# Optimization experiments

Hardware: AMD Instinct MI355X
Metric: run time of the kernel (lower is better)

Reference implementation:

```python
import jax, jax.numpy as jnp
import numpy as np

L = 6          # n_layers
V = 512        # vocab_size
D = 768        # n_embd == d_model
P = 768        # proj_size
H = 12         # num_heads
HD = P // H    # head dim = 64
FF = 4 * D     # MLP hidden = 3072
BLOCK = 1024   # block_size
B, T = 8, 1024
LN_EPS = 1e-5


def _layernorm(x, g, b):
    mu = jnp.mean(x, axis=-1, keepdims=True)
    var = jnp.mean(jnp.square(x - mu), axis=-1, keepdims=True)
    return (x - mu) * jax.lax.rsqrt(var + LN_EPS) * g + b


def setup_inputs() -> dict:
    key = jax.random.key(0)
    ks = iter(jax.random.split(key, 32))
    s = 0.02

    def rn(shape):
        return (jax.random.normal(next(ks), shape, jnp.float32) * s)

    inp = {
        "idx": jax.random.randint(next(ks), (B, T), 0, V),
        "attn_mask": jnp.ones((B, T), jnp.float32),
        "tok_emb": rn((V, D)),
        "pos_emb": rn((1, BLOCK, D)),
        # per-layer params stacked on leading L axis
        "ln1_g": jnp.ones((L, D)), "ln1_b": jnp.zeros((L, D)),
        "Wq": rn((L, D, P)), "bq": jnp.zeros((L, P)),
        "Wk": rn((L, D, P)), "bk": jnp.zeros((L, P)),
        "Wv": rn((L, D, P)), "bv": jnp.zeros((L, P)),
        "Wo": rn((L, P, D)), "bo": jnp.zeros((L, D)),
        "ln2_g": jnp.ones((L, D)), "ln2_b": jnp.zeros((L, D)),
        "W1": rn((L, D, FF)), "b1": jnp.zeros((L, FF)),
        "W2": rn((L, FF, D)), "b2": jnp.zeros((L, D)),
        "lnf_g": jnp.ones((D,)), "lnf_b": jnp.zeros((D,)),
        "W_out": rn((D, V)),  # logits head, no bias
    }
    return inp


def reference(idx, attn_mask, tok_emb, pos_emb, ln1_g, ln1_b, Wq, bq, Wk, bk,
              Wv, bv, Wo, bo, ln2_g, ln2_b, W1, b1, W2, b2, lnf_g, lnf_b, W_out):
    Bc, Tc = idx.shape
    x = tok_emb[idx] + pos_emb[:, :Tc]  # [B,T,D]  (dropout: eval mode, identity)

    tril = jnp.tril(jnp.ones((Tc, Tc), jnp.float32))
    # torch.minimum(look_ahead_mask, attn_mask.view(B,1,1,T))
    mask = jnp.minimum(tril[None, None], attn_mask[:, None, None, :])  # [B,1,T,T]
    neg_mask = mask == 0
    scale = 1.0 / np.sqrt(HD)

    layer_params = {
        "ln1_g": ln1_g, "ln1_b": ln1_b, "Wq": Wq, "bq": bq, "Wk": Wk, "bk": bk,
        "Wv": Wv, "bv": bv, "Wo": Wo, "bo": bo, "ln2_g": ln2_g, "ln2_b": ln2_b,
        "W1": W1, "b1": b1, "W2": W2, "b2": b2,
    }

    def block(x, p):
        h = _layernorm(x, p["ln1_g"], p["ln1_b"])
        q = (h @ p["Wq"] + p["bq"]).reshape(Bc, Tc, H, HD)
        k = (h @ p["Wk"] + p["bk"]).reshape(Bc, Tc, H, HD)
        v = (h @ p["Wv"] + p["bv"]).reshape(Bc, Tc, H, HD)
        att = jnp.einsum("bqhd,bkhd->bhqk", q, k) * scale
        att = jnp.where(neg_mask, -jnp.inf, att)
        w = jax.nn.softmax(att, axis=-1)  # attn dropout: identity in eval
        y = jnp.einsum("bhqk,bkhd->bqhd", w, v).reshape(Bc, Tc, P)
        x = x + (y @ p["Wo"] + p["bo"])
        h2 = _layernorm(x, p["ln2_g"], p["ln2_b"])
        m = jax.nn.gelu(h2 @ p["W1"] + p["b1"], approximate=False) @ p["W2"] + p["b2"]
        return x + m

    def step(x, p):
        return block(x, p), None

    x, _ = jax.lax.scan(step, x, layer_params)
    x = _layernorm(x, lnf_g, lnf_b)
    logits = x @ W_out  # [B,T,V]
    return logits
```

## Files before the change

### kernel.cpp

```cpp
#include <hip/hip_runtime.h>
#include <stdint.h>

#define LY 6
#define VOC 512
#define DM 768
#define NH 12
#define HD 64
#define FFD 3072
#define BB 8
#define TT 1024
#define ROWS (BB*TT)

typedef short bf16x8 __attribute__((ext_vector_type(8)));
typedef float f32x4 __attribute__((ext_vector_type(4)));
typedef unsigned short u16x4 __attribute__((ext_vector_type(4)));

__device__ __forceinline__ unsigned short f2bf(float f) {
    union { float f; uint32_t u; } v; v.f = f;
    uint32_t r = v.u + 0x7FFFu + ((v.u >> 16) & 1u);
    return (unsigned short)(r >> 16);
}

__device__ __forceinline__ void gl2lds16(const void* g, void* lds) {
    __builtin_amdgcn_global_load_lds(
        (const __attribute__((address_space(1))) uint32_t*)g,
        (__attribute__((address_space(3))) uint32_t*)lds,
        16, 0, 0);
}

__global__ void transpose_w(const float* __restrict__ src, unsigned short* __restrict__ dst,
                            int K, int N, long sls, long dls, int noff) {
    src += (long)blockIdx.z * sls;
    dst += (long)blockIdx.z * dls;
    const int k0 = blockIdx.y * 32, n0 = blockIdx.x * 32;
    __shared__ float tile[32][33];
    const int tx = threadIdx.x, ty = threadIdx.y;
#pragma unroll
    for (int i = 0; i < 4; ++i)
        tile[ty*4+i][tx] = src[(long)(k0 + ty*4 + i) * N + n0 + tx];
    __syncthreads();
#pragma unroll
    for (int i = 0; i < 4; ++i)
        dst[(long)(noff + n0 + ty*4 + i) * K + k0 + tx] = f2bf(tile[tx][ty*4+i]);
}

__global__ void pack_bqkv(const float* __restrict__ bq, const float* __restrict__ bk,
                          const float* __restrict__ bv, float* __restrict__ dst) {
    int i = blockIdx.x * 256 + threadIdx.x;
    if (i >= LY * 2304) return;
    int l = i / 2304, c = i % 2304;
    const float* s = (c < 768) ? bq : (c < 1536 ? bk : bv);
    dst[i] = s[l * 768 + (c % 768)];
}

__global__ __launch_bounds__(256) void embed_kernel(const int* __restrict__ idx,
        const float* __restrict__ tok, const float* __restrict__ pos, float* __restrict__ x) {
    const int g = blockIdx.x * 256 + threadIdx.x;
    const int row = g / 192, c = (g % 192) * 4;
    const int t = row & (TT - 1);
    const int tk = idx[row];
    const f32x4 a = *(const f32x4*)(tok + (long)tk * DM + c);
    const f32x4 p = *(const f32x4*)(pos + (long)t * DM + c);
    f32x4 o = a + p;
    *(f32x4*)(x + (long)row * DM + c) = o;
}

__global__ __launch_bounds__(256) void ln_kernel(const float* __restrict__ x,
        const float* __restrict__ gg, const float* __restrict__ bb,
        unsigned short* __restrict__ out) {
    const int row = (blockIdx.x * 256 + threadIdx.x) >> 6;
    const int lane = threadIdx.x & 63;
    const float* xr = x + (long)row * DM;
    f32x4 v[3];
#pragma unroll
    for (int i = 0; i < 3; ++i) v[i] = *(const f32x4*)(xr + i * 256 + lane * 4);
    float s = 0.f;
#pragma unroll
    for (int i = 0; i < 3; ++i) s += v[i][0] + v[i][1] + v[i][2] + v[i][3];
#pragma unroll
    for (int m = 1; m < 64; m <<= 1) s += __shfl_xor(s, m);
    const float mu = s * (1.f / 768.f);
    float q = 0.f;
#pragma unroll
    for (int i = 0; i < 3; ++i)
#pragma unroll
        for (int j = 0; j < 4; ++j) { float d = v[i][j] - mu; q += d * d; }
#pragma unroll
    for (int m = 1; m < 64; m <<= 1) q += __shfl_xor(q, m);
    const float rs = rsqrtf(q * (1.f / 768.f) + 1e-5f);
#pragma unroll
    for (int i = 0; i < 3; ++i) {
        u16x4 o;
#pragma unroll
        for (int j = 0; j < 4; ++j) {
            const int c = i * 256 + lane * 4 + j;
            o[j] = f2bf((v[i][j] - mu) * rs * gg[c] + bb[c]);
        }
        *(u16x4*)(out + (long)row * DM + i * 256 + lane * 4) = o;
    }
}

template <int EP>
__global__ __launch_bounds__(256)
void gemm128(const unsigned short* __restrict__ A, const unsigned short* __restrict__ Bt,
             const float* __restrict__ bias, const float* __restrict__ res,
             void* __restrict__ Cout, int M, int N, int K,
             unsigned short* __restrict__ aux) {
    __shared__ alignas(16) short As[128 * 64];
    __shared__ alignas(16) short Bs[128 * 64];
    const int tid = threadIdx.x;
    const int w = tid >> 6, lane = tid & 63, quad = lane >> 4, r = lane & 15;
    const int wm = w >> 1, wn = w & 1;
    const long rb = (long)blockIdx.x * 128;
    const long cb = (long)blockIdx.y * 128;

    f32x4 acc[4][4];
    const f32x4 z4 = {0.f, 0.f, 0.f, 0.f};
#pragma unroll
    for (int i = 0; i < 4; ++i)
#pragma unroll
        for (int j = 0; j < 4; ++j) acc[i][j] = z4;

    const int lrow = lane >> 3;
    const int lblk = (lane & 7) ^ lrow;

    for (int k0 = 0; k0 < K; k0 += 64) {
#pragma unroll
        for (int i = 0; i < 4; ++i) {
            const int c = i * 4 + w;
            gl2lds16(A + (rb + 8 * c + lrow) * (long)K + k0 + lblk * 8, (char*)As + c * 1024);
            gl2lds16(Bt + (cb + 8 * c + lrow) * (long)K + k0 + lblk * 8, (char*)Bs + c * 1024);
        }
        __builtin_amdgcn_s_waitcnt(0);
        __syncthreads();
#pragma unroll
        for (int kk = 0; kk < 2; ++kk) {
            bf16x8 af[4], bfr[4];
#pragma unroll
            for (int mi = 0; mi < 4; ++mi) {
                const int row = wm * 64 + mi * 16 + r;
                af[mi] = *(const bf16x8*)((const char*)As + row * 128 + (((kk * 4 + quad) ^ (row & 7)) * 16));
            }
#pragma unroll
            for (int ni = 0; ni < 4; ++ni) {
                const int col = wn * 64 + ni * 16 + r;
                bfr[ni] = *(const bf16x8*)((const char*)Bs + col * 128 + (((kk * 4 + quad) ^ (col & 7)) * 16));
            }
#pragma unroll
            for (int mi = 0; mi < 4; ++mi)
#pragma unroll
                for (int ni = 0; ni < 4; ++ni)
                    acc[mi][ni] = __builtin_amdgcn_mfma_f32_16x16x32_bf16(af[mi], bfr[ni], acc[mi][ni], 0, 0, 0);
        }
        __syncthreads();
    }

    if (EP == 4 && cb >= 1536) {
#pragma unroll
        for (int ni = 0; ni < 4; ++ni) {
            const int col = (int)cb + wn * 64 + ni * 16 + r;
            const float bv = bias[col];
            const int c = col - 1536, hh = c >> 6, dd = c & 63;
#pragma unroll
            for (int mi = 0; mi < 4; ++mi) {
                const int row0 = (int)rb + wm * 64 + mi * 16 + quad * 4;
                const int bb2 = row0 >> 10, t = row0 & 1023;
                u16x4 o;
#pragma unroll
                for (int reg = 0; reg < 4; ++reg) o[reg] = f2bf(acc[mi][ni][reg] + bv);
                *(u16x4*)(aux + (long)((bb2 * NH + hh) * 64 + dd) * TT + t) = o;
            }
        }
        return;
    }

#pragma unroll
    for (int ni = 0; ni < 4; ++ni) {
        const long col = cb + wn * 64 + ni * 16 + r;
        const float bv = (EP == 3) ? 0.f : bias[col];
#pragma unroll
        for (int mi = 0; mi < 4; ++mi) {
            const long row0 = rb + wm * 64 + mi * 16 + quad * 4;
#pragma unroll
            for (int reg = 0; reg < 4; ++reg) {
                const long off = (row0 + reg) * (long)N + col;
                float v = acc[mi][ni][reg] + bv;
                if (EP == 0 || EP == 4) {
                    ((unsigned short*)Cout)[off] = f2bf(v);
                } else if (EP == 1) {
                    v = 0.5f * v * (1.f + erff(v * 0.70710678118654752f));
                    ((unsigned short*)Cout)[off] = f2bf(v);
                } else if (EP == 2) {
                    ((float*)Cout)[off] = res[off] + v;
                } else {
                    ((float*)Cout)[off] = v;
                }
            }
        }
    }
}

__global__ __launch_bounds__(256)
void attn_kernel(const unsigned short* __restrict__ qkv, const unsigned short* __restrict__ vT,
                 const float* __restrict__ amask, unsigned short* __restrict__ y) {
    const int b = blockIdx.z, h = blockIdx.y, qb = blockIdx.x;
    const int q0 = qb * 128;
    const int tid = threadIdx.x, w = tid >> 6, lane = tid & 63, quad = lane >> 4, r = lane & 15;

    __shared__ alignas(16) short Ks[128 * 64];
    __shared__ alignas(16) short Vt[64 * 128];
    __shared__ alignas(16) short Pw[4][16 * 128];
    __shared__ float Msk[128];

    const float NINF = -__builtin_inff();
    const f32x4 z4 = {0.f, 0.f, 0.f, 0.f};

    bf16x8 qf[2][2];
#pragma unroll
    for (int qs = 0; qs < 2; ++qs)
#pragma unroll
        for (int ks = 0; ks < 2; ++ks)
            qf[qs][ks] = *(const bf16x8*)(qkv + (long)(b * TT + q0 + w * 32 + qs * 16 + r) * 2304
                                          + h * 64 + ks * 32 + quad * 8);

    f32x4 acc[2][4];
    float m_i[2] = {NINF, NINF}, l_i[2] = {0.f, 0.f};
#pragma unroll
    for (int qs = 0; qs < 2; ++qs)
#pragma unroll
        for (int dt = 0; dt < 4; ++dt) acc[qs][dt] = z4;

    short* Pme = &Pw[w][0];

    for (int kt = 0; kt <= qb; ++kt) {
#pragma unroll
        for (int i = 0; i < 4; ++i) {
            const int row = w * 32 + i * 8 + (lane >> 3);
            gl2lds16(qkv + (long)(b * TT + kt * 128 + row) * 2304 + 768 + h * 64
                         + (((lane & 7) ^ (row & 7)) << 3),
                     (char*)Ks + (w * 32 + i * 8) * 128);
        }
#pragma unroll
        for (int i = 0; i < 4; ++i) {
            const int drow = w * 16 + i * 4 + (lane >> 4);
            gl2lds16(vT + (long)((b * NH + h) * 64 + drow) * TT + kt * 128
                        + (((lane & 15) ^ (drow & 7)) << 3),
                     (char*)Vt + (w * 16 + i * 4) * 256);
        }
        if (tid < 128) Msk[tid] = amask[b * TT + kt * 128 + tid];
        __builtin_amdgcn_s_waitcnt(0);
        __syncthreads();

        const bool diag = (kt == qb);

        f32x4 s[2][8];
#pragma unroll
        for (int nt = 0; nt < 8; ++nt) {
            s[0][nt] = z4; s[1][nt] = z4;
#pragma unroll
            for (int ks = 0; ks < 2; ++ks) {
                const int krow = nt * 16 + r;
                const bf16x8 kf = *(const bf16x8*)((const char*)Ks + krow * 128
                                     + ((((ks << 2) + quad) ^ (krow & 7)) << 4));
                s[0][nt] = __builtin_amdgcn_mfma_f32_16x16x32_bf16(kf, qf[0][ks], s[0][nt], 0, 0, 0);
                s[1][nt] = __builtin_amdgcn_mfma_f32_16x16x32_bf16(kf, qf[1][ks], s[1][nt], 0, 0, 0);
            }
        }

#pragma unroll
        for (int qs = 0; qs < 2; ++qs) {
            const int qg = q0 + w * 32 + qs * 16 + r;
#pragma unroll
            for (int nt = 0; nt < 8; ++nt) {
                const f32x4 mk4 = *(const f32x4*)(Msk + nt * 16 + quad * 4);
#pragma unroll
                for (int reg = 0; reg < 4; ++reg) {
                    const int key = kt * 128 + nt * 16 + quad * 4 + reg;
                    const bool ok = (mk4[reg] != 0.f) && (!diag || key <= qg);
                    if (!ok) s[qs][nt][reg] = NINF;
                }
            }
            float mx = NINF;
#pragma unroll
            for (int nt = 0; nt < 8; ++nt)
                mx = fmaxf(mx, fmaxf(fmaxf(s[qs][nt][0], s[qs][nt][1]),
                                     fmaxf(s[qs][nt][2], s[qs][nt][3])));
            mx = fmaxf(mx, __shfl_xor(mx, 16));
            mx = fmaxf(mx, __shfl_xor(mx, 32));
            const float mnew = fmaxf(m_i[qs], mx);
            const float alpha = (m_i[qs] == NINF) ? 0.f : __expf((m_i[qs] - mnew) * 0.125f);
            m_i[qs] = mnew;

            float rs = 0.f;
#pragma unroll
            for (int nt = 0; nt < 8; ++nt) {
                u16x4 pk;
#pragma unroll
                for (int reg = 0; reg < 4; ++reg) {
                    const float p = (s[qs][nt][reg] == NINF)
                                  ? 0.f : __expf((s[qs][nt][reg] - mnew) * 0.125f);
                    rs += p;
                    pk[reg] = f2bf(p);
                }
                const int kblk = nt * 2 + (quad >> 1);
                *(u16x4*)(Pme + r * 128 + ((kblk ^ (r & 7)) << 3) + ((quad & 1) << 2)) = pk;
            }
            rs += __shfl_xor(rs, 16);
            rs += __shfl_xor(rs, 32);
            l_i[qs] = l_i[qs] * alpha + rs;

            float al[4];
#pragma unroll
            for (int reg = 0; reg < 4; ++reg)
                al[reg] = __shfl(alpha, (lane & 48) + quad * 4 + reg);
#pragma unroll
            for (int dt = 0; dt < 4; ++dt)
#pragma unroll
                for (int reg = 0; reg < 4; ++reg)
                    acc[qs][dt][reg] *= al[reg];

#pragma unroll
            for (int kk = 0; kk < 4; ++kk) {
                const bf16x8 pf = *(const bf16x8*)(Pme + r * 128
                                     + ((((kk << 2) + quad) ^ (r & 7)) << 3));
#pragma unroll
                for (int dt = 0; dt < 4; ++dt) {
                    const int dd = dt * 16 + r;
                    const bf16x8 vf = *(const bf16x8*)((const char*)Vt + dd * 256
                                        + ((((kk << 2) + quad) ^ (dd & 7)) << 4));
                    acc[qs][dt] = __builtin_amdgcn_mfma_f32_16x16x32_bf16(pf, vf, acc[qs][dt], 0, 0, 0);
                }
            }
        }
        __syncthreads();
    }

#pragma unroll
    for (int qs = 0; qs < 2; ++qs) {
        const float inv0 = 1.0f / l_i[qs];
#pragma unroll
        for (int reg = 0; reg < 4; ++reg) {
            const float inv = __shfl(inv0, (lane & 48) + quad * 4 + reg);
            const long row = b * TT + q0 + w * 32 + qs * 16 + quad * 4 + reg;
#pragma unroll
            for (int dt = 0; dt < 4; ++dt)
                y[row * DM + h * 64 + dt * 16 + r] = f2bf(acc[qs][dt][reg] * inv);
        }
    }
}

extern "C" void kernel_launch(void* const* d_in, const int* in_sizes, int n_in,
                              void* d_out, int out_size, void* d_ws, size_t ws_size,
                              hipStream_t stream) {
    (void)in_sizes; (void)n_in; (void)out_size; (void)ws_size;
    const int*   idx   = (const int*)d_in[0];
    const float* amask = (const float*)d_in[1];
    const float* tok   = (const float*)d_in[2];
    const float* pos   = (const float*)d_in[3];
    const float* ln1g  = (const float*)d_in[4];
    const float* ln1b  = (const float*)d_in[5];
    const float* Wq    = (const float*)d_in[6];
    const float* bq    = (const float*)d_in[7];
    const float* Wk    = (const float*)d_in[8];
    const float* bk    = (const float*)d_in[9];
    const float* Wv    = (const float*)d_in[10];
    const float* bv    = (const float*)d_in[11];
    const float* Wo    = (const float*)d_in[12];
    const float* bo    = (const float*)d_in[13];
    const float* ln2g  = (const float*)d_in[14];
    const float* ln2b  = (const float*)d_in[15];
    const float* W1    = (const float*)d_in[16];
    const float* b1    = (const float*)d_in[17];
    const float* W2    = (const float*)d_in[18];
    const float* b2    = (const float*)d_in[19];
    const float* lnfg  = (const float*)d_in[20];
    const float* lnfb  = (const float*)d_in[21];
    const float* Wout  = (const float*)d_in[22];

    char* ws = (char*)d_ws;
    float* x            = (float*)ws;          ws += (size_t)ROWS * DM * 4;
    unsigned short* h   = (unsigned short*)ws; ws += (size_t)ROWS * DM * 2;
    unsigned short* qkv = (unsigned short*)ws; ws += (size_t)ROWS * 2304 * 2;
    unsigned short* vT  = (unsigned short*)ws; ws += (size_t)ROWS * DM * 2;
    unsigned short* y   = (unsigned short*)ws; ws += (size_t)ROWS * DM * 2;
    unsigned short* m1  = (unsigned short*)ws; ws += (size_t)ROWS * FFD * 2;
    unsigned short* qkvT= (unsigned short*)ws; ws += (size_t)LY * 2304 * DM * 2;
    unsigned short* WoT = (unsigned short*)ws; ws += (size_t)LY * DM * DM * 2;
    unsigned short* W1T = (unsigned short*)ws; ws += (size_t)LY * FFD * DM * 2;
    unsigned short* W2T = (unsigned short*)ws; ws += (size_t)LY * DM * FFD * 2;
    unsigned short* WouT= (unsigned short*)ws; ws += (size_t)VOC * DM * 2;
    float* bqkv         = (float*)ws;          ws += (size_t)LY * 2304 * 4;

    dim3 blk32(32, 8, 1);
    transpose_w<<<dim3(24, 24, LY), blk32, 0, stream>>>(Wq, qkvT, 768, 768, 768L*768, 2304L*768, 0);
    transpose_w<<<dim3(24, 24, LY), blk32, 0, stream>>>(Wk, qkvT, 768, 768, 768L*768, 2304L*768, 768);
    transpose_w<<<dim3(24, 24, LY), blk32, 0, stream>>>(Wv, qkvT, 768, 768, 768L*768, 2304L*768, 1536);
    transpose_w<<<dim3(24, 24, LY), blk32, 0, stream>>>(Wo, WoT, 768, 768, 768L*768, 768L*768, 0);
    transpose_w<<<dim3(96, 24, LY), blk32, 0, stream>>>(W1, W1T, 768, 3072, 768L*3072, 3072L*768, 0);
    transpose_w<<<dim3(24, 96, LY), blk32, 0, stream>>>(W2, W2T, 3072, 768, 3072L*768, 768L*3072, 0);
    transpose_w<<<dim3(16, 24, 1),  blk32, 0, stream>>>(Wout, WouT, 768, 512, 768L*512, 512L*768, 0);
    pack_bqkv<<<dim3(54), 256, 0, stream>>>(bq, bk, bv, bqkv);
    embed_kernel<<<dim3(6144), 256, 0, stream>>>(idx, tok, pos, x);

    for (int l = 0; l < LY; ++l) {
        ln_kernel<<<2048, 256, 0, stream>>>(x, ln1g + l * DM, ln1b + l * DM, h);
        gemm128<4><<<dim3(64, 18), 256, 0, stream>>>(h, qkvT + (size_t)l * 2304 * DM, bqkv + l * 2304,
                                                     nullptr, qkv, ROWS, 2304, DM, vT);
        attn_kernel<<<dim3(8, NH, BB), 256, 0, stream>>>(qkv, vT, amask, y);
        gemm128<2><<<dim3(64, 6), 256, 0, stream>>>(y, WoT + (size_t)l * DM * DM, bo + l * DM,
                                                    x, x, ROWS, DM, DM, nullptr);
        ln_kernel<<<2048, 256, 0, stream>>>(x, ln2g + l * DM, ln2b + l * DM, h);
        gemm128<1><<<dim3(64, 24), 256, 0, stream>>>(h, W1T + (size_t)l * FFD * DM, b1 + l * FFD,
                                                     nullptr, m1, ROWS, FFD, DM, nullptr);
        gemm128<2><<<dim3(64, 6), 256, 0, stream>>>(m1, W2T + (size_t)l * DM * FFD, b2 + l * DM,
                                                    x, x, ROWS, DM, FFD, nullptr);
    }
    ln_kernel<<<2048, 256, 0, stream>>>(x, lnfg, lnfb, h);
    gemm128<3><<<dim3(64, 4), 256, 0, stream>>>(h, WouT, nullptr, nullptr, d_out, ROWS, VOC, DM, nullptr);
}
```

Before: 2.205 ms.

## Restructure attention into per-wave 32-row strips with register K/V loads

Rewrites the attention kernel so each wave independently processes a 32-query strip over 32-key tiles. K and V fragments load straight from global memory into registers, with K prefetched one tile ahead, instead of going through LDS with block-wide barriers. Strips are interleaved across waves (strip = w*8 + blockIdx.y) to balance the causal workload, and softmax uses exp2 with the scale folded into an FMA together with an additive mask bias. This removes __syncthreads and shared K/V staging at the cost of redundant global loads across waves and smaller MFMA tiles per iteration.

```diff
diff --git a/kernel.cpp b/kernel.cpp
--- a/kernel.cpp
+++ b/kernel.cpp
@@ -15,10 +15,21 @@
 typedef float f32x4 __attribute__((ext_vector_type(4)));
 typedef unsigned short u16x4 __attribute__((ext_vector_type(4)));
 
+#if __has_builtin(__builtin_amdgcn_exp2f)
+#define EXP2 __builtin_amdgcn_exp2f
+#else
+#define EXP2 exp2f
+#endif
+
 __device__ __forceinline__ unsigned short f2bf(float f) {
     union { float f; uint32_t u; } v; v.f = f;
     uint32_t r = v.u + 0x7FFFu + ((v.u >> 16) & 1u);
     return (unsigned short)(r >> 16);
+}
+
+__device__ __forceinline__ uint32_t f2u(float f) {
+    union { float f; uint32_t u; } v; v.f = f;
+    return v.u;
 }
 
 __device__ __forceinline__ void gl2lds16(const void* g, void* lds) {
@@ -200,17 +211,114 @@
     }
 }
 
-__global__ __launch_bounds__(256)
+#define C1S 0.18033688011112042f
+
+#define LOADK(KT, KF)                                                                     \
+    {                                                                                     \
+        const unsigned short* kg_ = qkv + (long)(b * TT + (KT) * 32 + r) * 2304           \
+                                    + 768 + h * 64 + quad * 8;                            \
+        KF[0][0] = *(const bf16x8*)(kg_);                                                 \
+        KF[0][1] = *(const bf16x8*)(kg_ + 32);                                            \
+        KF[1][0] = *(const bf16x8*)(kg_ + 16 * 2304);                                     \
+        KF[1][1] = *(const bf16x8*)(kg_ + 16 * 2304 + 32);                                \
+    }
+
+#define PROCESS(KT, KF, KFN)                                                              \
+    {                                                                                     \
+        const int kt_ = (KT);                                                             \
+        const unsigned short* vg_ = vT + (long)(bh * 64 + r) * TT + kt_ * 32 + quad * 8;  \
+        bf16x8 vf_[4];                                                                    \
+        vf_[0] = *(const bf16x8*)(vg_);                                                   \
+        vf_[1] = *(const bf16x8*)(vg_ + 16 * TT);                                         \
+        vf_[2] = *(const bf16x8*)(vg_ + 32 * TT);                                         \
+        vf_[3] = *(const bf16x8*)(vg_ + 48 * TT);                                         \
+        const f32x4 mk0_ = *(const f32x4*)(amask + b * TT + kt_ * 32 + quad * 4);         \
+        const f32x4 mk1_ = *(const f32x4*)(amask + b * TT + kt_ * 32 + 16 + quad * 4);    \
+        if (kt_ < strip) LOADK(kt_ + 1, KFN);                                             \
+        f32x4 st_[2][2];                                                                  \
+        _Pragma("unroll")                                                                 \
+        for (int qs = 0; qs < 2; ++qs) {                                                  \
+            _Pragma("unroll")                                                             \
+            for (int nt = 0; nt < 2; ++nt) {                                              \
+                st_[qs][nt] = z4;                                                         \
+                st_[qs][nt] = __builtin_amdgcn_mfma_f32_16x16x32_bf16(KF[nt][0], qf[qs][0], st_[qs][nt], 0, 0, 0); \
+                st_[qs][nt] = __builtin_amdgcn_mfma_f32_16x16x32_bf16(KF[nt][1], qf[qs][1], st_[qs][nt], 0, 0, 0); \
+            }                                                                             \
+        }                                                                                 \
+        f32x4 mb0_, mb1_;                                                                 \
+        _Pragma("unroll")                                                                 \
+        for (int j = 0; j < 4; ++j) {                                                     \
+            mb0_[j] = (mk0_[j] == 0.f) ? NINF : 0.f;                                      \
+            mb1_[j] = (mk1_[j] == 0.f) ? NINF : 0.f;                                      \
+        }                                                                                 \
+        const bool diag_ = (kt_ == strip);                                                \
+        _Pragma("unroll")                                                                 \
+        for (int qs = 0; qs < 2; ++qs) {                                                  \
+            f32x4 t0_, t1_;                                                               \
+            _Pragma("unroll")                                                             \
+            for (int j = 0; j < 4; ++j) {                                                 \
+                t0_[j] = fmaf(st_[qs][0][j], C1S, mb0_[j]);                               \
+                t1_[j] = fmaf(st_[qs][1][j], C1S, mb1_[j]);                               \
+            }                                                                             \
+            if (diag_) {                                                                  \
+                const int qg_ = qs * 16 + r;                                              \
+                _Pragma("unroll")                                                         \
+                for (int j = 0; j < 4; ++j) {                                             \
+                    if (quad * 4 + j > qg_)      t0_[j] = NINF;                           \
+                    if (16 + quad * 4 + j > qg_) t1_[j] = NINF;                           \
+                }                                                                         \
+            }                                                                             \
+            float mx_ = fmaxf(fmaxf(fmaxf(t0_[0], t0_[1]), fmaxf(t0_[2], t0_[3])),        \
+                              fmaxf(fmaxf(t1_[0], t1_[1]), fmaxf(t1_[2], t1_[3])));       \
+            mx_ = fmaxf(mx_, __shfl_xor(mx_, 16));                                        \
+            mx_ = fmaxf(mx_, __shfl_xor(mx_, 32));                                        \
+            const float mnew_ = fmaxf(m_i[qs], mx_);                                      \
+            const float alpha_ = EXP2(m_i[qs] - mnew_);                                   \
+            m_i[qs] = mnew_;                                                              \
+            f32x4 p0_, p1_;                                                               \
+            _Pragma("unroll")                                                             \
+            for (int j = 0; j < 4; ++j) {                                                 \
+                p0_[j] = EXP2(t0_[j] - mnew_);                                            \
+                p1_[j] = EXP2(t1_[j] - mnew_);                                            \
+            }                                                                             \
+            float rs_ = ((p0_[0] + p0_[1]) + (p0_[2] + p0_[3]))                           \
+                      + ((p1_[0] + p1_[1]) + (p1_[2] + p1_[3]));                          \
+            rs_ += __shfl_xor(rs_, 16);                                                   \
+            rs_ += __shfl_xor(rs_, 32);                                                   \
+            l_i[qs] = l_i[qs] * alpha_ + rs_;                                             \
+            short* Pq_ = Pb + qs * 512;                                                   \
+            const uint2 w0_ = { __builtin_amdgcn_perm(f2u(p0_[1]), f2u(p0_[0]), 0x07060302), \
+                                __builtin_amdgcn_perm(f2u(p0_[3]), f2u(p0_[2]), 0x07060302) }; \
+            const uint2 w1_ = { __builtin_amdgcn_perm(f2u(p1_[1]), f2u(p1_[0]), 0x07060302), \
+                                __builtin_amdgcn_perm(f2u(p1_[3]), f2u(p1_[2]), 0x07060302) }; \
+            const int half_ = (quad & 1) * 4;                                             \
+            *(uint2*)(Pq_ + r * 32 + ((((quad >> 1)) ^ (r & 3)) << 3) + half_) = w0_;     \
+            *(uint2*)(Pq_ + r * 32 + (((2 + (quad >> 1)) ^ (r & 3)) << 3) + half_) = w1_; \
+            float al_[4];                                                                 \
+            _Pragma("unroll")                                                             \
+            for (int reg = 0; reg < 4; ++reg)                                             \
+                al_[reg] = __shfl(alpha_, (lane & 48) | (quad * 4 + reg));                \
+            _Pragma("unroll")                                                             \
+            for (int dt = 0; dt < 4; ++dt)                                                \
+                _Pragma("unroll")                                                         \
+                for (int reg = 0; reg < 4; ++reg) acc[qs][dt][reg] *= al_[reg];           \
+            const bf16x8 pf_ = *(const bf16x8*)(Pq_ + r * 32 + ((quad ^ (r & 3)) << 3));  \
+            _Pragma("unroll")                                                             \
+            for (int dt = 0; dt < 4; ++dt)                                                \
+                acc[qs][dt] = __builtin_amdgcn_mfma_f32_16x16x32_bf16(pf_, vf_[dt], acc[qs][dt], 0, 0, 0); \
+        }                                                                                 \
+    }
+
+__global__ __launch_bounds__(256, 3)
 void attn_kernel(const unsigned short* __restrict__ qkv, const unsigned short* __restrict__ vT,
                  const float* __restrict__ amask, unsigned short* __restrict__ y) {
-    const int b = blockIdx.z, h = blockIdx.y, qb = blockIdx.x;
-    const int q0 = qb * 128;
+    const int bh = blockIdx.x, b = bh / NH, h = bh % NH;
     const int tid = threadIdx.x, w = tid >> 6, lane = tid & 63, quad = lane >> 4, r = lane & 15;
-
-    __shared__ alignas(16) short Ks[128 * 64];
-    __shared__ alignas(16) short Vt[64 * 128];
-    __shared__ alignas(16) short Pw[4][16 * 128];
-    __shared__ float Msk[128];
+    const int strip = w * 8 + blockIdx.y;
+    const int q0 = strip * 32;
+
+    __shared__ alignas(16) short Pall[4 * 2 * 512];
+    short* Pb = Pall + w * 1024;
 
     const float NINF = -__builtin_inff();
     const f32x4 z4 = {0.f, 0.f, 0.f, 0.f};
@@ -220,7 +328,7 @@
     for (int qs = 0; qs < 2; ++qs)
 #pragma unroll
         for (int ks = 0; ks < 2; ++ks)
-            qf[qs][ks] = *(const bf16x8*)(qkv + (long)(b * TT + q0 + w * 32 + qs * 16 + r) * 2304
+            qf[qs][ks] = *(const bf16x8*)(qkv + (long)(b * TT + q0 + qs * 16 + r) * 2304
                                           + h * 64 + ks * 32 + quad * 8);
 
     f32x4 acc[2][4];
@@ -230,109 +338,14 @@
 #pragma unroll
         for (int dt = 0; dt < 4; ++dt) acc[qs][dt] = z4;
 
-    short* Pme = &Pw[w][0];
-
-    for (int kt = 0; kt <= qb; ++kt) {
-#pragma unroll
-        for (int i = 0; i < 4; ++i) {
-            const int row = w * 32 + i * 8 + (lane >> 3);
-            gl2lds16(qkv + (long)(b * TT + kt * 128 + row) * 2304 + 768 + h * 64
-                         + (((lane & 7) ^ (row & 7)) << 3),
-                     (char*)Ks + (w * 32 + i * 8) * 128);
-        }
-#pragma unroll
-        for (int i = 0; i < 4; ++i) {
-            const int drow = w * 16 + i * 4 + (lane >> 4);
-            gl2lds16(vT + (long)((b * NH + h) * 64 + drow) * TT + kt * 128
-                        + (((lane & 15) ^ (drow & 7)) << 3),
-                     (char*)Vt + (w * 16 + i * 4) * 256);
-        }
-        if (tid < 128) Msk[tid] = amask[b * TT + kt * 128 + tid];
-        __builtin_amdgcn_s_waitcnt(0);
-        __syncthreads();
-
-        const bool diag = (kt == qb);
-
-        f32x4 s[2][8];
-#pragma unroll
-        for (int nt = 0; nt < 8; ++nt) {
-            s[0][nt] = z4; s[1][nt] = z4;
-#pragma unroll
-            for (int ks = 0; ks < 2; ++ks) {
-                const int krow = nt * 16 + r;
-                const bf16x8 kf = *(const bf16x8*)((const char*)Ks + krow * 128
-                                     + ((((ks << 2) + quad) ^ (krow & 7)) << 4));
-                s[0][nt] = __builtin_amdgcn_mfma_f32_16x16x32_bf16(kf, qf[0][ks], s[0][nt], 0, 0, 0);
-                s[1][nt] = __builtin_amdgcn_mfma_f32_16x16x32_bf16(kf, qf[1][ks], s[1][nt], 0, 0, 0);
-            }
-        }
-
-#pragma unroll
-        for (int qs = 0; qs < 2; ++qs) {
-            const int qg = q0 + w * 32 + qs * 16 + r;
-#pragma unroll
-            for (int nt = 0; nt < 8; ++nt) {
-                const f32x4 mk4 = *(const f32x4*)(Msk + nt * 16 + quad * 4);
-#pragma unroll
-                for (int reg = 0; reg < 4; ++reg) {
-                    const int key = kt * 128 + nt * 16 + quad * 4 + reg;
-                    const bool ok = (mk4[reg] != 0.f) && (!diag || key <= qg);
-                    if (!ok) s[qs][nt][reg] = NINF;
-                }
-            }
-            float mx = NINF;
-#pragma unroll
-            for (int nt = 0; nt < 8; ++nt)
-                mx = fmaxf(mx, fmaxf(fmaxf(s[qs][nt][0], s[qs][nt][1]),
-                                     fmaxf(s[qs][nt][2], s[qs][nt][3])));
-            mx = fmaxf(mx, __shfl_xor(mx, 16));
-            mx = fmaxf(mx, __shfl_xor(mx, 32));
-            const float mnew = fmaxf(m_i[qs], mx);
-            const float alpha = (m_i[qs] == NINF) ? 0.f : __expf((m_i[qs] - mnew) * 0.125f);
-            m_i[qs] = mnew;
-
-            float rs = 0.f;
-#pragma unroll
-            for (int nt = 0; nt < 8; ++nt) {
-                u16x4 pk;
-#pragma unroll
-                for (int reg = 0; reg < 4; ++reg) {
-                    const float p = (s[qs][nt][reg] == NINF)
-                                  ? 0.f : __expf((s[qs][nt][reg] - mnew) * 0.125f);
-                    rs += p;
-                    pk[reg] = f2bf(p);
-                }
-                const int kblk = nt * 2 + (quad >> 1);
-                *(u16x4*)(Pme + r * 128 + ((kblk ^ (r & 7)) << 3) + ((quad & 1) << 2)) = pk;
-            }
-            rs += __shfl_xor(rs, 16);
-            rs += __shfl_xor(rs, 32);
-            l_i[qs] = l_i[qs] * alpha + rs;
-
-            float al[4];
-#pragma unroll
-            for (int reg = 0; reg < 4; ++reg)
-                al[reg] = __shfl(alpha, (lane & 48) + quad * 4 + reg);
-#pragma unroll
-            for (int dt = 0; dt < 4; ++dt)
-#pragma unroll
-                for (int reg = 0; reg < 4; ++reg)
-                    acc[qs][dt][reg] *= al[reg];
-
-#pragma unroll
-            for (int kk = 0; kk < 4; ++kk) {
-                const bf16x8 pf = *(const bf16x8*)(Pme + r * 128
-                                     + ((((kk << 2) + quad) ^ (r & 7)) << 3));
-#pragma unroll
-                for (int dt = 0; dt < 4; ++dt) {
-                    const int dd = dt * 16 + r;
-                    const bf16x8 vf = *(const bf16x8*)((const char*)Vt + dd * 256
-                                        + ((((kk << 2) + quad) ^ (dd & 7)) << 4));
-                    acc[qs][dt] = __builtin_amdgcn_mfma_f32_16x16x32_bf16(pf, vf, acc[qs][dt], 0, 0, 0);
-                }
-            }
-        }
-        __syncthreads();
+    bf16x8 kfA[2][2], kfB[2][2];
+    LOADK(0, kfA);
+    int kt = 0;
+    for (;;) {
+        PROCESS(kt, kfA, kfB);
+        ++kt; if (kt > strip) break;
+        PROCESS(kt, kfB, kfA);
+        ++kt; if (kt > strip) break;
     }
 
 #pragma unroll
@@ -340,8 +353,8 @@
         const float inv0 = 1.0f / l_i[qs];
 #pragma unroll
         for (int reg = 0; reg < 4; ++reg) {
-            const float inv = __shfl(inv0, (lane & 48) + quad * 4 + reg);
-            const long row = b * TT + q0 + w * 32 + qs * 16 + quad * 4 + reg;
+            const float inv = __shfl(inv0, (lane & 48) | (quad * 4 + reg));
+            const long row = b * TT + q0 + qs * 16 + quad * 4 + reg;
 #pragma unroll
             for (int dt = 0; dt < 4; ++dt)
                 y[row * DM + h * 64 + dt * 16 + r] = f2bf(acc[qs][dt][reg] * inv);
@@ -406,7 +419,7 @@
         ln_kernel<<<2048, 256, 0, stream>>>(x, ln1g + l * DM, ln1b + l * DM, h);
         gemm128<4><<<dim3(64, 18), 256, 0, stream>>>(h, qkvT + (size_t)l * 2304 * DM, bqkv + l * 2304,
                                                      nullptr, qkv, ROWS, 2304, DM, vT);
-        attn_kernel<<<dim3(8, NH, BB), 256, 0, stream>>>(qkv, vT, amask, y);
+        attn_kernel<<<dim3(96, 8), 256, 0, stream>>>(qkv, vT, amask, y);
         gemm128<2><<<dim3(64, 6), 256, 0, stream>>>(y, WoT + (size_t)l * DM * DM, bo + l * DM,
                                                     x, x, ROWS, DM, DM, nullptr);
         ln_kernel<<<2048, 256, 0, stream>>>(x, ln2g + l * DM, ln2b + l * DM, h);
```

New measurement: 1.976 ms. -10.4%, faster.
